# Optimization experiments

Measured on AMD Instinct MI355X. Metric: run time of the kernel, lower is better.

Reference implementation:

```python
import jax, jax.numpy as jnp
import numpy as np

VOCAB_SIZE = 1024
EMBED_DIM = 64
Z_SHAPE = (64, 32, 32, EMBED_DIM)


def setup_inputs() -> dict:
    key = jax.random.key(0)
    kz, kc = jax.random.split(key)
    z = jax.random.normal(kz, Z_SHAPE, dtype=jnp.float32)
    codebook = jax.random.uniform(kc, (VOCAB_SIZE, EMBED_DIM), dtype=jnp.float32)
    return {"z": z, "codebook": codebook}


def reference(z, codebook):
    # Flatten all leading dims: [N, D]
    z_flat = jnp.reshape(z, (-1, EMBED_DIM))
    # Squared euclidean distance via expansion: |z|^2 + |c|^2 - 2 z.c
    d1 = jnp.sum(z_flat ** 2, axis=1, keepdims=True)      # [N, 1]
    d2 = jnp.sum(codebook ** 2, axis=1)                   # [V]
    d3 = 2.0 * jnp.dot(z_flat, codebook.T)                # [N, V]
    distances = d1 + d2 - d3                              # [N, V]
    tokens = jnp.argmin(distances, axis=1)                # [N]
    tokens = jnp.reshape(tokens, z.shape[:-1])            # [B, H, W]
    z_quantized = codebook[tokens]                        # [B, H, W, D]
    return (z_quantized, tokens, codebook)
```

## Files before the change

### kernel.cpp

```cpp
#include <hip/hip_runtime.h>
#include <float.h>

constexpr int D     = 64;
constexpr int V     = 1024;
constexpr int NROWS = 65536;
constexpr float MARGIN = 0.01f;

typedef _Float16 half8 __attribute__((ext_vector_type(8)));
typedef float    f32x4 __attribute__((ext_vector_type(4)));

__global__ __launch_bounds__(256) void vq_prep(
    const float* __restrict__ cb, _Float16* __restrict__ wsH,
    _Float16* __restrict__ wsL, float* __restrict__ c2,
    float* __restrict__ cbout, int* __restrict__ cnt) {
  const int gid = blockIdx.x * 256 + threadIdx.x;
  if (gid == 0) cnt[0] = 0;

  ((float4*)cbout)[gid] = ((const float4*)cb)[gid];

  if (gid < V) {
    const int cw = gid;
    const float* src = cb + (size_t)cw * D;
    float part = 0.f;
#pragma unroll
    for (int chunk = 0; chunk < 8; ++chunk) {
      float4 q0 = ((const float4*)(src + chunk * 8))[0];
      float4 q1 = ((const float4*)(src + chunk * 8))[1];
      float xs[8] = {q0.x, q0.y, q0.z, q0.w, q1.x, q1.y, q1.z, q1.w};
      half8 hh, hl;
#pragma unroll
      for (int e = 0; e < 8; ++e) {
        _Float16 hi = (_Float16)xs[e];
        hh[e] = hi;
        hl[e] = (_Float16)(xs[e] - (float)hi);
        part  = fmaf(xs[e], xs[e], part);
      }
      *(half8*)&wsH[((size_t)chunk * V + cw) * 8] = hh;
      *(half8*)&wsL[((size_t)chunk * V + cw) * 8] = hl;
    }
    c2[cw] = part;
  }
}

__global__ __launch_bounds__(256, 4) void vq_screen(
    const float* __restrict__ z, const float* __restrict__ cb,
    const _Float16* __restrict__ wsH, const _Float16* __restrict__ wsL,
    const float* __restrict__ c2g,
    float* __restrict__ zq, float* __restrict__ tok,
    int* __restrict__ cnt, int* __restrict__ list) {
  __shared__ __align__(16) _Float16 sBh[2][8][64][8];
  __shared__ __align__(16) _Float16 sBl[2][8][64][8];
  __shared__ __align__(16) float sC2a[1024];
  __shared__ int   sW[4][16];
  __shared__ int   sFlagRows[64];
  __shared__ int   sFlagCnt, sFlagBase;

  const int tid  = threadIdx.x;
  const int lane = tid & 63;
  const int wv   = tid >> 6;
  const int l15  = lane & 15;
  const int quad = lane >> 4;
  const int gw   = blockIdx.x * 4 + wv;
  const int rowbase = gw * 16;

  if (tid == 0) sFlagCnt = 0;

  half8 afh[2], afl[2];
  {
    const float* zr = z + (size_t)(rowbase + l15) * D;
#pragma unroll
    for (int h = 0; h < 2; ++h) {
      const float4* p = (const float4*)(zr + h * 32 + quad * 8);
      float4 q0 = p[0], q1 = p[1];
      float xs[8] = {q0.x, q0.y, q0.z, q0.w, q1.x, q1.y, q1.z, q1.w};
      half8 ah, al;
#pragma unroll
      for (int e = 0; e < 8; ++e) {
        _Float16 hi = (_Float16)xs[e];
        ah[e] = hi;
        al[e] = (_Float16)(xs[e] - (float)hi);
      }
      afh[h] = ah; afl[h] = al;
    }
  }

  float b1[4], b2[4]; int i1[4];
#pragma unroll
  for (int r = 0; r < 4; ++r) { b1[r] = FLT_MAX; b2[r] = FLT_MAX; i1[r] = 0; }

  {
    float4 qc = ((const float4*)c2g)[tid];
    *(float4*)&sC2a[tid * 4] = qc;
  }
#pragma unroll
  for (int i = 0; i < 4; ++i) {
    const int idx   = i * 256 + tid;
    const int seg   = idx >> 6;
    const int off   = idx & 63;
    const int chunk = seg & 7;
    const _Float16* srcb = (seg < 8) ? wsH : wsL;
    const half8 v = *(const half8*)&srcb[((size_t)chunk * V + off) * 8];
    if (seg < 8) *(half8*)&sBh[0][chunk][off][0] = v;
    else         *(half8*)&sBl[0][chunk][off][0] = v;
  }
  __syncthreads();

  for (int hp = 0; hp < 16; ++hp) {
    const int cur = hp & 1;
    const int nxt = cur ^ 1;
    half8 pre[4];
    if (hp < 15) {
#pragma unroll
      for (int i = 0; i < 4; ++i) {
        const int idx   = i * 256 + tid;
        const int seg   = idx >> 6;
        const int off   = idx & 63;
        const int chunk = seg & 7;
        const _Float16* srcb = (seg < 8) ? wsH : wsL;
        pre[i] = *(const half8*)&srcb[((size_t)chunk * V + (hp + 1) * 64 + off) * 8];
      }
    }
#pragma unroll
    for (int tl = 0; tl < 4; ++tl) {
      const int cwl  = tl * 16 + l15;
      const int vcol = hp * 64 + cwl;
      const float c2v = sC2a[hp * 64 + cwl];
      half8 bh0 = *(const half8*)&sBh[cur][quad][cwl][0];
      half8 bh1 = *(const half8*)&sBh[cur][4 + quad][cwl][0];
      half8 bl0 = *(const half8*)&sBl[cur][quad][cwl][0];
      half8 bl1 = *(const half8*)&sBl[cur][4 + quad][cwl][0];
      f32x4 acc1 = {0.f, 0.f, 0.f, 0.f};
      f32x4 acc2 = {0.f, 0.f, 0.f, 0.f};
      acc1 = __builtin_amdgcn_mfma_f32_16x16x32_f16(afh[0], bh0, acc1, 0, 0, 0);
      acc2 = __builtin_amdgcn_mfma_f32_16x16x32_f16(afh[1], bh1, acc2, 0, 0, 0);
      acc1 = __builtin_amdgcn_mfma_f32_16x16x32_f16(afh[0], bl0, acc1, 0, 0, 0);
      acc2 = __builtin_amdgcn_mfma_f32_16x16x32_f16(afh[1], bl1, acc2, 0, 0, 0);
      acc1 = __builtin_amdgcn_mfma_f32_16x16x32_f16(afl[0], bh0, acc1, 0, 0, 0);
      acc2 = __builtin_amdgcn_mfma_f32_16x16x32_f16(afl[1], bh1, acc2, 0, 0, 0);
#pragma unroll
      for (int r = 0; r < 4; ++r) {
        float m0 = fmaf(-2.f, acc1[r] + acc2[r], c2v);
        bool  c0 = m0 < b1[r];
        b2[r] = __builtin_amdgcn_fmed3f(m0, b1[r], b2[r]);
        b1[r] = fminf(b1[r], m0);
        i1[r] = c0 ? vcol : i1[r];
      }
    }
    if (hp < 15) {
#pragma unroll
      for (int i = 0; i < 4; ++i) {
        const int idx   = i * 256 + tid;
        const int seg   = idx >> 6;
        const int off   = idx & 63;
        const int chunk = seg & 7;
        if (seg < 8) *(half8*)&sBh[nxt][chunk][off][0] = pre[i];
        else         *(half8*)&sBl[nxt][chunk][off][0] = pre[i];
      }
    }
    __syncthreads();
  }

#pragma unroll
  for (int r = 0; r < 4; ++r) {
    float v1 = b1[r], v2 = b2[r]; int ix = i1[r];
#pragma unroll
    for (int s = 1; s < 16; s <<= 1) {
      float ov1 = __shfl_xor(v1, s);
      float ov2 = __shfl_xor(v2, s);
      int   oix = __shfl_xor(ix, s);
      bool take = (ov1 < v1) || (ov1 == v1 && oix < ix);
      float worse = take ? v1 : ov1;
      v2 = fminf(fminf(v2, ov2), worse);
      v1 = take ? ov1 : v1;
      ix = take ? oix : ix;
    }
    b1[r] = v1; b2[r] = v2; i1[r] = ix;
  }

  if (l15 == 0) {
#pragma unroll
    for (int r = 0; r < 4; ++r) {
      int rl = quad * 4 + r;
      sW[wv][rl] = i1[r];
      if (b2[r] - b1[r] < MARGIN) {
        int s = atomicAdd(&sFlagCnt, 1);
        sFlagRows[s] = rowbase + rl;
      }
    }
  }
  __syncthreads();
  if (tid == 0 && sFlagCnt > 0) sFlagBase = atomicAdd(cnt, sFlagCnt);
  __syncthreads();
  if (tid < sFlagCnt) list[sFlagBase + tid] = sFlagRows[tid];

  if (tid < 64) tok[blockIdx.x * 64 + tid] = (float)sW[tid >> 4][tid & 15];

#pragma unroll
  for (int i = 0; i < 4; ++i) {
    int cid = i * 256 + tid;
    int r = cid >> 4, seg = cid & 15;
    int widx = sW[r >> 4][r & 15];
    float4 val = *(const float4*)(cb + (size_t)widx * D + seg * 4);
    *(float4*)(zq + (size_t)(blockIdx.x * 64 + r) * D + seg * 4) = val;
  }
}

__global__ __launch_bounds__(256) void vq_fallback(
    const float* __restrict__ z, const float* __restrict__ cb,
    const int* __restrict__ cnt, const int* __restrict__ list,
    float* __restrict__ zq, float* __restrict__ tok) {
  __shared__ float sv[256];
  __shared__ int   si[256];
  const int t = threadIdx.x;
  const int n = cnt[0];
  for (int it = blockIdx.x; it < n; it += gridDim.x) {
    int row = __builtin_amdgcn_readfirstlane(list[it]);
    const float* zr = z + (size_t)row * D;
    float zreg[D];
#pragma unroll
    for (int i = 0; i < D / 4; ++i) {
      float4 q = ((const float4*)zr)[i];
      zreg[4 * i] = q.x; zreg[4 * i + 1] = q.y; zreg[4 * i + 2] = q.z; zreg[4 * i + 3] = q.w;
    }
    float d1 = 0.f;
#pragma unroll
    for (int i = 0; i < D; ++i) d1 = fmaf(zreg[i], zreg[i], d1);
    float best = FLT_MAX; int bidx = 0;
    for (int c = 0; c < 4; ++c) {
      int v = t + 256 * c;
      const float* cp = cb + (size_t)v * D;
      float acc = 0.f, cc = 0.f;
#pragma unroll
      for (int dd = 0; dd < D; ++dd) {
        acc = fmaf(zreg[dd], cp[dd], acc);
        cc  = fmaf(cp[dd], cp[dd], cc);
      }
      float dist = (d1 + cc) - 2.f * acc;
      if (dist < best) { best = dist; bidx = v; }
    }
    sv[t] = best; si[t] = bidx;
    __syncthreads();
    for (int s = 128; s > 0; s >>= 1) {
      if (t < s) {
        float v2 = sv[t + s]; int i2 = si[t + s];
        if (v2 < sv[t] || (v2 == sv[t] && i2 < si[t])) { sv[t] = v2; si[t] = i2; }
      }
      __syncthreads();
    }
    int win = si[0];
    if (t == 0) tok[row] = (float)win;
    if (t < 16) {
      float4 q = ((const float4*)(cb + (size_t)win * D))[t];
      ((float4*)(zq + (size_t)row * D))[t] = q;
    }
    __syncthreads();
  }
}

extern "C" void kernel_launch(void* const* d_in, const int* in_sizes, int n_in,
                              void* d_out, int out_size, void* d_ws, size_t ws_size,
                              hipStream_t stream) {
  const float* z  = (const float*)d_in[0];
  const float* cb = (const float*)d_in[1];

  float* out = (float*)d_out;
  float* zq  = out;
  float* tok = out + (size_t)NROWS * D;
  float* cbo = tok + NROWS;

  char* wsb = (char*)d_ws;
  _Float16* wsH  = (_Float16*)(wsb + 0);
  _Float16* wsL  = (_Float16*)(wsb + 131072);
  float*    c2   = (float*)(wsb + 262144);
  int*      cnt  = (int*)(wsb + 266240);
  int*      list = (int*)(wsb + 266496);

  vq_prep<<<64, 256, 0, stream>>>(cb, wsH, wsL, c2, cbo, cnt);
  vq_screen<<<1024, 256, 0, stream>>>(z, cb, wsH, wsL, c2, zq, tok, cnt, list);
  vq_fallback<<<1024, 256, 0, stream>>>(z, cb, cnt, list, zq, tok);
}
```

Before: 128.9 us.

## Widen screen blocks to 8 waves and use shuffle reduction in fallback

The screening kernel now runs 512-thread blocks covering 128 rows, so each codebook tile staged into shared memory is reused by twice as many waves, halving total L2-to-LDS traffic and per-thread prefetch registers. The fallback kernel replaces its shared-memory tree reduction with wave shuffles plus a small cross-wave step, cutting barriers per flagged row. Larger blocks halve the grid, which may reduce occupancy flexibility and tail balance. __launch_bounds__(512,4) may also tighten the register budget.

```diff
diff --git a/kernel.cpp b/kernel.cpp
--- a/kernel.cpp
+++ b/kernel.cpp
@@ -42,7 +42,7 @@
   }
 }
 
-__global__ __launch_bounds__(256, 4) void vq_screen(
+__global__ __launch_bounds__(512, 4) void vq_screen(
     const float* __restrict__ z, const float* __restrict__ cb,
     const _Float16* __restrict__ wsH, const _Float16* __restrict__ wsL,
     const float* __restrict__ c2g,
@@ -51,8 +51,8 @@
   __shared__ __align__(16) _Float16 sBh[2][8][64][8];
   __shared__ __align__(16) _Float16 sBl[2][8][64][8];
   __shared__ __align__(16) float sC2a[1024];
-  __shared__ int   sW[4][16];
-  __shared__ int   sFlagRows[64];
+  __shared__ int   sW[8][16];
+  __shared__ int   sFlagRows[128];
   __shared__ int   sFlagCnt, sFlagBase;
 
   const int tid  = threadIdx.x;
@@ -60,7 +60,7 @@
   const int wv   = tid >> 6;
   const int l15  = lane & 15;
   const int quad = lane >> 4;
-  const int gw   = blockIdx.x * 4 + wv;
+  const int gw   = blockIdx.x * 8 + wv;
   const int rowbase = gw * 16;
 
   if (tid == 0) sFlagCnt = 0;
@@ -89,12 +89,12 @@
   for (int r = 0; r < 4; ++r) { b1[r] = FLT_MAX; b2[r] = FLT_MAX; i1[r] = 0; }
 
   {
-    float4 qc = ((const float4*)c2g)[tid];
-    *(float4*)&sC2a[tid * 4] = qc;
-  }
-#pragma unroll
-  for (int i = 0; i < 4; ++i) {
-    const int idx   = i * 256 + tid;
+    float2 qc = ((const float2*)c2g)[tid];
+    *(float2*)&sC2a[tid * 2] = qc;
+  }
+#pragma unroll
+  for (int i = 0; i < 2; ++i) {
+    const int idx   = i * 512 + tid;
     const int seg   = idx >> 6;
     const int off   = idx & 63;
     const int chunk = seg & 7;
@@ -108,11 +108,11 @@
   for (int hp = 0; hp < 16; ++hp) {
     const int cur = hp & 1;
     const int nxt = cur ^ 1;
-    half8 pre[4];
+    half8 pre[2];
     if (hp < 15) {
 #pragma unroll
-      for (int i = 0; i < 4; ++i) {
-        const int idx   = i * 256 + tid;
+      for (int i = 0; i < 2; ++i) {
+        const int idx   = i * 512 + tid;
         const int seg   = idx >> 6;
         const int off   = idx & 63;
         const int chunk = seg & 7;
@@ -148,8 +148,8 @@
     }
     if (hp < 15) {
 #pragma unroll
-      for (int i = 0; i < 4; ++i) {
-        const int idx   = i * 256 + tid;
+      for (int i = 0; i < 2; ++i) {
+        const int idx   = i * 512 + tid;
         const int seg   = idx >> 6;
         const int off   = idx & 63;
         const int chunk = seg & 7;
@@ -193,15 +193,15 @@
   __syncthreads();
   if (tid < sFlagCnt) list[sFlagBase + tid] = sFlagRows[tid];
 
-  if (tid < 64) tok[blockIdx.x * 64 + tid] = (float)sW[tid >> 4][tid & 15];
+  if (tid < 128) tok[blockIdx.x * 128 + tid] = (float)sW[tid >> 4][tid & 15];
 
 #pragma unroll
   for (int i = 0; i < 4; ++i) {
-    int cid = i * 256 + tid;
+    int cid = i * 512 + tid;
     int r = cid >> 4, seg = cid & 15;
     int widx = sW[r >> 4][r & 15];
     float4 val = *(const float4*)(cb + (size_t)widx * D + seg * 4);
-    *(float4*)(zq + (size_t)(blockIdx.x * 64 + r) * D + seg * 4) = val;
+    *(float4*)(zq + (size_t)(blockIdx.x * 128 + r) * D + seg * 4) = val;
   }
 }
 
@@ -209,9 +209,12 @@
     const float* __restrict__ z, const float* __restrict__ cb,
     const int* __restrict__ cnt, const int* __restrict__ list,
     float* __restrict__ zq, float* __restrict__ tok) {
-  __shared__ float sv[256];
-  __shared__ int   si[256];
+  __shared__ float sRv[4];
+  __shared__ int   sRi[4];
+  __shared__ int   sWin;
   const int t = threadIdx.x;
+  const int wv = t >> 6;
+  const int ln = t & 63;
   const int n = cnt[0];
   for (int it = blockIdx.x; it < n; it += gridDim.x) {
     int row = __builtin_amdgcn_readfirstlane(list[it]);
@@ -236,19 +239,28 @@
         cc  = fmaf(cp[dd], cp[dd], cc);
       }
       float dist = (d1 + cc) - 2.f * acc;
-      if (dist < best) { best = dist; bidx = v; }
-    }
-    sv[t] = best; si[t] = bidx;
-    __syncthreads();
-    for (int s = 128; s > 0; s >>= 1) {
-      if (t < s) {
-        float v2 = sv[t + s]; int i2 = si[t + s];
-        if (v2 < sv[t] || (v2 == sv[t] && i2 < si[t])) { sv[t] = v2; si[t] = i2; }
-      }
-      __syncthreads();
-    }
-    int win = si[0];
-    if (t == 0) tok[row] = (float)win;
+      if (dist < best || (dist == best && v < bidx)) { best = dist; bidx = v; }
+    }
+#pragma unroll
+    for (int s = 1; s < 64; s <<= 1) {
+      float ov = __shfl_xor(best, s);
+      int   oi = __shfl_xor(bidx, s);
+      if (ov < best || (ov == best && oi < bidx)) { best = ov; bidx = oi; }
+    }
+    if (ln == 0) { sRv[wv] = best; sRi[wv] = bidx; }
+    __syncthreads();
+    if (t == 0) {
+      float bv = sRv[0]; int bi = sRi[0];
+#pragma unroll
+      for (int w = 1; w < 4; ++w) {
+        float ov = sRv[w]; int oi = sRi[w];
+        if (ov < bv || (ov == bv && oi < bi)) { bv = ov; bi = oi; }
+      }
+      sWin = bi;
+      tok[row] = (float)bi;
+    }
+    __syncthreads();
+    int win = sWin;
     if (t < 16) {
       float4 q = ((const float4*)(cb + (size_t)win * D))[t];
       ((float4*)(zq + (size_t)row * D))[t] = q;
@@ -276,6 +288,6 @@
   int*      list = (int*)(wsb + 266496);
 
   vq_prep<<<64, 256, 0, stream>>>(cb, wsH, wsL, c2, cbo, cnt);
-  vq_screen<<<1024, 256, 0, stream>>>(z, cb, wsH, wsL, c2, zq, tok, cnt, list);
+  vq_screen<<<512, 512, 0, stream>>>(z, cb, wsH, wsL, c2, zq, tok, cnt, list);
   vq_fallback<<<1024, 256, 0, stream>>>(z, cb, cnt, list, zq, tok);
 }
```

New measurement: 251.8 us. 1.95x slower.
